# Kernel tuning notes

Hardware: AMD Instinct MI355X
Metric: run time of the kernel (lower is better)

The kernel has to match this reference:

```python
import jax, jax.numpy as jnp
import numpy as np

QUERY = 1024
VALUE = 1024
HID = 1024
SEQ = 2048
BATCH = 64
INIT_RANGE = 0.1


def setup_inputs() -> dict:
    key = jax.random.key(0)
    ks = jax.random.split(key, 5)
    q = jax.random.normal(ks[0], (BATCH, QUERY), dtype=jnp.float32)
    v = jax.random.normal(ks[1], (SEQ, BATCH, VALUE), dtype=jnp.float32)
    u = lambda k, shape: jax.random.uniform(k, shape, jnp.float32, -INIT_RANGE, INIT_RANGE)
    W_v = u(ks[2], (HID, VALUE))
    b_v = jnp.zeros((HID,), jnp.float32)
    W_q = u(ks[3], (HID, QUERY))
    b_q = jnp.zeros((HID,), jnp.float32)
    W_o = u(ks[4], (1, HID))
    b_o = jnp.zeros((1,), jnp.float32)
    return {"q": q, "v": v, "W_v": W_v, "b_v": b_v, "W_q": W_q, "b_q": b_q, "W_o": W_o, "b_o": b_o}


def reference(q, v, W_v, b_v, W_q, b_q, W_o, b_o):
    # v: [S, B, V] -> [B, S, V]
    vt = jnp.transpose(v, (1, 0, 2))
    h_v = jnp.einsum('bsv,hv->bsh', vt, W_v) + b_v          # [B, S, H]
    h_q = jnp.einsum('bq,hq->bh', q, W_q) + b_q              # [B, H]
    h = jnp.tanh(h_v + h_q[:, None, :])                      # [B, S, H]
    logit = jnp.einsum('bsh,h->bs', h, W_o[0]) + b_o[0]      # [B, S]
    logit = logit - jnp.max(logit, axis=1, keepdims=True)
    p = jax.nn.softmax(logit, axis=1)                        # [B, S]
    ctx = jnp.sum(vt * p[:, :, None], axis=1, keepdims=True) # [B, 1, V]
    out = jnp.transpose(ctx, (1, 0, 2))                      # [1, B, V]
    return (out, p)
```

## Files before the change

### kernel.cpp

```cpp
#include <hip/hip_runtime.h>
#include <hip/hip_bf16.h>
#include <stdint.h>

#define BATCH 64
#define SEQ   2048
#define VDIM  1024
#define HDIM  1024
#define LDSB  24576

typedef __bf16 b8v __attribute__((ext_vector_type(8)));
typedef __bf16 b4v __attribute__((ext_vector_type(4)));
typedef float f32x4 __attribute__((ext_vector_type(4)));
typedef unsigned short u16x8 __attribute__((ext_vector_type(8)));

__device__ __forceinline__ float bf2f(unsigned short u) {
    union { unsigned int i; float f; } cv; cv.i = ((unsigned int)u) << 16; return cv.f;
}

__device__ __forceinline__ unsigned int pack_bf16_2(float a, float b) {
#if __has_builtin(__builtin_amdgcn_cvt_pk_bf16_f32)
    auto t = __builtin_amdgcn_cvt_pk_bf16_f32(a, b);
    unsigned int r; __builtin_memcpy(&r, &t, 4); return r;
#else
    union { float f; unsigned int u; } ca, cb; ca.f = a; cb.f = b;
    unsigned int ra = ca.u + 0x7FFF + ((ca.u >> 16) & 1);
    unsigned int rb = cb.u + 0x7FFF + ((cb.u >> 16) & 1);
    return (ra >> 16) | (rb & 0xFFFF0000u);
#endif
}

__device__ __forceinline__ void gload_lds16(const unsigned short* g, unsigned short* l) {
    __builtin_amdgcn_global_load_lds(
        (const __attribute__((address_space(1))) unsigned int*)g,
        (__attribute__((address_space(3))) unsigned int*)l, 16, 0, 0);
}

__global__ __launch_bounds__(256) void cvt_bf16_kernel(
    const float* __restrict__ in, unsigned short* __restrict__ out, long n8)
{
    long g = (long)blockIdx.x * 256 + threadIdx.x;
    if (g >= n8) return;
    float4 a = *(const float4*)(in + g * 8);
    float4 b = *(const float4*)(in + g * 8 + 4);
    b8v o = {(__bf16)a.x, (__bf16)a.y, (__bf16)a.z, (__bf16)a.w,
             (__bf16)b.x, (__bf16)b.y, (__bf16)b.z, (__bf16)b.w};
    *(b8v*)(out + g * 8) = o;
}

__global__ __launch_bounds__(256) void hq_kernel(
    const float* __restrict__ q, const float* __restrict__ Wq,
    const float* __restrict__ bq, const float* __restrict__ bv,
    float* __restrict__ hq)
{
    const int h = blockIdx.x * 4 + (threadIdx.x >> 6);
    const int lane = threadIdx.x & 63;
    const float4* qr = (const float4*)(q + ((size_t)lane << 10));
    const float4* wr = (const float4*)(Wq + ((size_t)h << 10));
    float acc = 0.f;
    #pragma unroll 8
    for (int k = 0; k < 256; ++k) {
        float4 wa = wr[k];
        float4 qa = qr[k];
        acc += qa.x*wa.x + qa.y*wa.y + qa.z*wa.z + qa.w*wa.w;
    }
    hq[((size_t)lane << 10) + h] = acc + bq[h] + bv[h];
}

__global__ __launch_bounds__(512, 2) void fused_8ph(
    const unsigned short* __restrict__ v, const unsigned short* __restrict__ Wv,
    const float* __restrict__ Wo, const float* __restrict__ hq,
    float* __restrict__ logit)
{
    __shared__ __align__(16) unsigned short lds[3 * LDSB];
    __shared__ float logit_lds[128];

    const int tid  = threadIdx.x;
    const int w    = tid >> 6;
    const int lane = tid & 63;
    const int col  = lane & 15;
    const int quad = lane >> 4;
    const int wm   = w >> 2;
    const int wn   = w & 3;

    const int bid    = blockIdx.x;
    const int work   = ((bid & 7) << 9) + (bid >> 3);
    const int m_tile = work >> 2;
    const int n_tile = work & 3;

    if (tid < 128) logit_lds[tid] = 0.f;

    f32x4 acc[4][4];
    #pragma unroll
    for (int i = 0; i < 4; ++i)
        #pragma unroll
        for (int j = 0; j < 4; ++j) acc[i][j] = (f32x4)(0.f);

    const int rowoff = tid >> 3;
    const int ch     = (tid & 7) ^ (rowoff & 7);
    const unsigned short* gA = v  + (size_t)(m_tile * 128 + rowoff) * VDIM + (ch << 3);
    const unsigned short* gB = Wv + (size_t)(n_tile * 256 + rowoff) * VDIM + (ch << 3);
    const int ldA = tid << 3;
    const int ldB = 8192 + (tid << 3);

    gload_lds16(gA,                  lds + ldA);
    gload_lds16(gA + 64*VDIM,        lds + 4096 + ldA);
    gload_lds16(gB,                  lds + ldB);
    gload_lds16(gB + 64*VDIM,        lds + 4096 + ldB);
    gload_lds16(gB + 128*VDIM,       lds + 8192 + ldB);
    gload_lds16(gB + 192*VDIM,       lds + 12288 + ldB);
    gload_lds16(gA + 64,             lds + LDSB + ldA);
    gload_lds16(gA + 64 + 64*VDIM,   lds + LDSB + 4096 + ldA);
    gload_lds16(gB + 64,             lds + LDSB + ldB);
    gload_lds16(gB + 64 + 64*VDIM,   lds + LDSB + 4096 + ldB);
    gload_lds16(gB + 64 + 128*VDIM,  lds + LDSB + 8192 + ldB);
    gload_lds16(gB + 64 + 192*VDIM,  lds + LDSB + 12288 + ldB);
    asm volatile("s_waitcnt vmcnt(6)" ::: "memory");
    __builtin_amdgcn_s_barrier();

    const int aoffbase = (wm * 64 + col) * 64;
    const int boffbase = 8192 + (wn * 64 + col) * 64;
    const int axor     = col & 7;

    const unsigned short* gAs = gA + 128;
    const unsigned short* gBs = gB + 128;
    int cbase = 0;
    int sbase = 2 * LDSB;

    b8v aF[4], bF[4];

#define FRAG_LOAD(kkc)                                                          \
    {   const int co = ((((kkc) << 2) + quad) ^ axor) << 3;                     \
        _Pragma("unroll") for (int i = 0; i < 4; ++i)                           \
            aF[i] = *(const b8v*)(lds + cbase + aoffbase + i*1024 + co);        \
        _Pragma("unroll") for (int j = 0; j < 4; ++j)                           \
            bF[j] = *(const b8v*)(lds + cbase + boffbase + j*1024 + co);    }

#define MFMA16()                                                                \
    _Pragma("unroll") for (int i = 0; i < 4; ++i)                               \
        _Pragma("unroll") for (int j = 0; j < 4; ++j)                           \
            acc[i][j] = __builtin_amdgcn_mfma_f32_16x16x32_bf16(aF[i], bF[j], acc[i][j], 0, 0, 0);

    #pragma unroll 1
    for (int t = 0; t < 16; ++t) {
        FRAG_LOAD(0)
        if (t < 14) {
            gload_lds16(gAs,            lds + sbase + ldA);
            gload_lds16(gAs + 64*VDIM,  lds + sbase + 4096 + ldA);
            gload_lds16(gBs,            lds + sbase + ldB);
        }
        __builtin_amdgcn_s_barrier();
        asm volatile("s_waitcnt lgkmcnt(0)" ::: "memory");
        __builtin_amdgcn_sched_barrier(0);
        __builtin_amdgcn_s_setprio(1);
        MFMA16()
        __builtin_amdgcn_s_setprio(0);
        __builtin_amdgcn_s_barrier();

        FRAG_LOAD(1)
        if (t < 14) {
            gload_lds16(gBs + 64*VDIM,   lds + sbase + 4096 + ldB);
            gload_lds16(gBs + 128*VDIM,  lds + sbase + 8192 + ldB);
            gload_lds16(gBs + 192*VDIM,  lds + sbase + 12288 + ldB);
        }
        __builtin_amdgcn_s_barrier();
        asm volatile("s_waitcnt lgkmcnt(0)" ::: "memory");
        __builtin_amdgcn_sched_barrier(0);
        __builtin_amdgcn_s_setprio(1);
        MFMA16()
        __builtin_amdgcn_s_setprio(0);
        if (t <= 13)      { asm volatile("s_waitcnt vmcnt(6)" ::: "memory"); }
        else if (t == 14) { asm volatile("s_waitcnt vmcnt(0)" ::: "memory"); }
        __builtin_amdgcn_s_barrier();

        gAs += 64; gBs += 64;
        cbase += LDSB; if (cbase == 3 * LDSB) cbase = 0;
        sbase += LDSB; if (sbase == 3 * LDSB) sbase = 0;
    }
#undef FRAG_LOAD
#undef MFMA16

    float rowsum[4][4];
    #pragma unroll
    for (int i = 0; i < 4; ++i)
        #pragma unroll
        for (int r = 0; r < 4; ++r) rowsum[i][r] = 0.f;
    #pragma unroll
    for (int j = 0; j < 4; ++j) {
        const int h = n_tile * 256 + wn * 64 + j * 16 + col;
        const float wo = Wo[h];
        #pragma unroll
        for (int i = 0; i < 4; ++i) {
            const int brow = i * 16 + quad * 4;
            #pragma unroll
            for (int r = 0; r < 4; ++r) {
                float x = acc[i][j][r] + hq[(brow + r) * HDIM + h];
                float t = __expf(2.f * x);
                rowsum[i][r] += wo * (1.f - 2.f / (t + 1.f));
            }
        }
    }
    #pragma unroll
    for (int off = 1; off < 16; off <<= 1)
        #pragma unroll
        for (int i = 0; i < 4; ++i)
            #pragma unroll
            for (int r = 0; r < 4; ++r)
                rowsum[i][r] += __shfl_xor(rowsum[i][r], off, 64);
    if (col == 0) {
        #pragma unroll
        for (int i = 0; i < 4; ++i)
            #pragma unroll
            for (int r = 0; r < 4; ++r)
                atomicAdd(&logit_lds[wm * 64 + i * 16 + quad * 4 + r], rowsum[i][r]);
    }
    __syncthreads();
    if (tid < 128) {
        const int b = tid & 63;
        const int s = m_tile * 2 + (tid >> 6);
        atomicAdd(&logit[b * SEQ + s], logit_lds[tid]);
    }
}

#define GEMM_EPILOGUE()                                                        \
    float rowsum[4][4];                                                        \
    _Pragma("unroll") for (int i = 0; i < 4; ++i)                              \
        _Pragma("unroll") for (int r = 0; r < 4; ++r) rowsum[i][r] = 0.f;      \
    _Pragma("unroll") for (int j = 0; j < 4; ++j) {                            \
        const int h = n_tile*128 + wave_n + j*16 + col;                        \
        const float wo = Wo[h];                                                \
        _Pragma("unroll") for (int i = 0; i < 4; ++i) {                        \
            const int brow = i*16 + quad*4;                                    \
            _Pragma("unroll") for (int r = 0; r < 4; ++r) {                    \
                float x = acc[i][j][r] + hq[(brow + r)*HDIM + h];              \
                float t = __expf(2.f * x);                                     \
                rowsum[i][r] += wo * (1.f - 2.f / (t + 1.f));                  \
            }                                                                  \
        }                                                                      \
    }                                                                          \
    _Pragma("unroll") for (int off = 1; off < 16; off <<= 1)                   \
        _Pragma("unroll") for (int i = 0; i < 4; ++i)                          \
            _Pragma("unroll") for (int r = 0; r < 4; ++r)                      \
                rowsum[i][r] += __shfl_xor(rowsum[i][r], off, 64);             \
    if (col == 0) {                                                            \
        _Pragma("unroll") for (int i = 0; i < 4; ++i)                          \
            _Pragma("unroll") for (int r = 0; r < 4; ++r)                      \
                atomicAdd(&logit_lds[wave_m + i*16 + quad*4 + r], rowsum[i][r]); \
    }                                                                          \
    __syncthreads();                                                           \
    if (tid < 128) {                                                           \
        const int b = tid & 63;                                                \
        const int s = m_tile*2 + (tid >> 6);                                   \
        atomicAdd(&logit[b*SEQ + s], logit_lds[tid]);                          \
    }

__global__ __launch_bounds__(256) void fused_f32(
    const float* __restrict__ v, const float* __restrict__ Wv,
    const float* __restrict__ Wo, const float* __restrict__ hq,
    float* __restrict__ logit)
{
    __shared__ __align__(16) unsigned short ldsA[128*32];
    __shared__ __align__(16) unsigned short ldsB[128*32];
    __shared__ float logit_lds[128];

    const int tid  = threadIdx.x;
    const int w    = tid >> 6;
    const int lane = tid & 63;
    const int col  = lane & 15;
    const int quad = lane >> 4;
    const int wave_m = (w >> 1) << 6;
    const int wave_n = (w & 1) << 6;
    const int n_tile = blockIdx.x;
    const int m_tile = blockIdx.y;

    if (tid < 128) logit_lds[tid] = 0.f;

    f32x4 acc[4][4];
    #pragma unroll
    for (int i = 0; i < 4; ++i)
        #pragma unroll
        for (int j = 0; j < 4; ++j) acc[i][j] = (f32x4)(0.f);

    const int srow8 = lane >> 3;
    const int scolf = (lane & 7) << 2;
    const float* gA = v  + (size_t)(m_tile * 128 + w*32 + srow8) * VDIM + scolf;
    const float* gB = Wv + (size_t)(n_tile * 128 + w*32 + srow8) * VDIM + scolf;
    unsigned short* lA = ldsA + (w*32 + srow8)*32 + ((lane & 7) << 2);
    unsigned short* lB = ldsB + (w*32 + srow8)*32 + ((lane & 7) << 2);

    float4 ra[4], rb[4];
    #pragma unroll
    for (int r = 0; r < 4; ++r) {
        ra[r] = *(const float4*)(gA + r*8*VDIM);
        rb[r] = *(const float4*)(gB + r*8*VDIM);
    }

    for (int kt = 0; kt < 32; ++kt) {
        __syncthreads();
        #pragma unroll
        for (int r = 0; r < 4; ++r) {
            uint2 pa = { pack_bf16_2(ra[r].x, ra[r].y), pack_bf16_2(ra[r].z, ra[r].w) };
            uint2 pb = { pack_bf16_2(rb[r].x, rb[r].y), pack_bf16_2(rb[r].z, rb[r].w) };
            *(uint2*)(lA + r*256) = pa;
            *(uint2*)(lB + r*256) = pb;
        }
        __syncthreads();

        if (kt < 31) {
            const int ko = (kt + 1) << 5;
            #pragma unroll
            for (int r = 0; r < 4; ++r) {
                ra[r] = *(const float4*)(gA + ko + r*8*VDIM);
                rb[r] = *(const float4*)(gB + ko + r*8*VDIM);
            }
        }

        b8v aF[4], bF[4];
        #pragma unroll
        for (int i = 0; i < 4; ++i)
            aF[i] = *(const b8v*)(ldsA + ((wave_m + i*16 + col) << 5) + (quad << 3));
        #pragma unroll
        for (int j = 0; j < 4; ++j)
            bF[j] = *(const b8v*)(ldsB + ((wave_n + j*16 + col) << 5) + (quad << 3));
        #pragma unroll
        for (int i = 0; i < 4; ++i)
            #pragma unroll
            for (int j = 0; j < 4; ++j)
                acc[i][j] = __builtin_amdgcn_mfma_f32_16x16x32_bf16(aF[i], bF[j], acc[i][j], 0, 0, 0);
    }

    GEMM_EPILOGUE()
}

__global__ __launch_bounds__(256) void softmax_kernel(float* __restrict__ logit,
                                                      float* __restrict__ pout)
{
    const int b = blockIdx.x, tid = threadIdx.x;
    float* row = logit + b * SEQ;
    __shared__ float red[4];

    float e[8];
    float lmax = -1e30f;
    #pragma unroll
    for (int k = 0; k < 8; ++k) { e[k] = row[tid + k*256]; lmax = fmaxf(lmax, e[k]); }
    #pragma unroll
    for (int off = 32; off > 0; off >>= 1) lmax = fmaxf(lmax, __shfl_xor(lmax, off, 64));
    if ((tid & 63) == 0) red[tid >> 6] = lmax;
    __syncthreads();
    lmax = fmaxf(fmaxf(red[0], red[1]), fmaxf(red[2], red[3]));
    __syncthreads();
    float lsum = 0.f;
    #pragma unroll
    for (int k = 0; k < 8; ++k) { e[k] = __expf(e[k] - lmax); lsum += e[k]; }
    #pragma unroll
    for (int off = 32; off > 0; off >>= 1) lsum += __shfl_xor(lsum, off, 64);
    if ((tid & 63) == 0) red[tid >> 6] = lsum;
    __syncthreads();
    lsum = red[0] + red[1] + red[2] + red[3];
    const float inv = 1.f / lsum;
    #pragma unroll
    for (int k = 0; k < 8; ++k) {
        const int s = tid + k*256;
        const float pv = e[k] * inv;
        row[s] = pv;
        pout[b*SEQ + s] = pv;
    }
}

__global__ __launch_bounds__(128) void ctx_f32(
    const float* __restrict__ v, const float* __restrict__ p, float* __restrict__ ctx)
{
    const int b = blockIdx.y, sc = blockIdx.x, tid = threadIdx.x;
    float acc[8];
    #pragma unroll
    for (int e = 0; e < 8; ++e) acc[e] = 0.f;
    for (int s = sc*128; s < sc*128 + 128; ++s) {
        const float pv = p[b*SEQ + s];
        const float4* vp = (const float4*)(v + (size_t)(s*64 + b) * VDIM + tid*8);
        float4 v0 = vp[0], v1 = vp[1];
        acc[0] = fmaf(pv, v0.x, acc[0]); acc[1] = fmaf(pv, v0.y, acc[1]);
        acc[2] = fmaf(pv, v0.z, acc[2]); acc[3] = fmaf(pv, v0.w, acc[3]);
        acc[4] = fmaf(pv, v1.x, acc[4]); acc[5] = fmaf(pv, v1.y, acc[5]);
        acc[6] = fmaf(pv, v1.z, acc[6]); acc[7] = fmaf(pv, v1.w, acc[7]);
    }
    #pragma unroll
    for (int e = 0; e < 8; ++e) atomicAdd(&ctx[b*VDIM + tid*8 + e], acc[e]);
}

__global__ __launch_bounds__(128) void ctx_bf16(
    const unsigned short* __restrict__ v, const float* __restrict__ p, float* __restrict__ ctx)
{
    const int b = blockIdx.y, sc = blockIdx.x, tid = threadIdx.x;
    float acc[8];
    #pragma unroll
    for (int e = 0; e < 8; ++e) acc[e] = 0.f;
    for (int s = sc*128; s < sc*128 + 128; ++s) {
        const float pv = p[b*SEQ + s];
        u16x8 val = *(const u16x8*)(v + (size_t)(s*64 + b) * VDIM + tid*8);
        #pragma unroll
        for (int e = 0; e < 8; ++e) acc[e] = fmaf(pv, bf2f(val[e]), acc[e]);
    }
    #pragma unroll
    for (int e = 0; e < 8; ++e) atomicAdd(&ctx[b*VDIM + tid*8 + e], acc[e]);
}

extern "C" void kernel_launch(void* const* d_in, const int* in_sizes, int n_in,
                              void* d_out, int out_size, void* d_ws, size_t ws_size,
                              hipStream_t stream)
{
    const float* q  = (const float*)d_in[0];
    const float* v  = (const float*)d_in[1];
    const float* Wv = (const float*)d_in[2];
    const float* bv = (const float*)d_in[3];
    const float* Wq = (const float*)d_in[4];
    const float* bq = (const float*)d_in[5];
    const float* Wo = (const float*)d_in[6];

    float* hq_ws    = (float*)d_ws;
    float* logit_ws = hq_ws + 65536;
    float* ctx_ws   = logit_ws + 131072;
    unsigned short* vb  = (unsigned short*)(ctx_ws + 65536);
    unsigned short* Wvb = vb + (size_t)SEQ*BATCH*VDIM;

    const size_t needA = (size_t)(65536 + 131072 + 65536) * 4
                       + ((size_t)SEQ*BATCH*VDIM + (size_t)HDIM*VDIM) * 2;
    const bool bigws = ws_size >= needA;

    float* out_ctx = (float*)d_out;
    float* out_p   = out_ctx + 65536;

    hipMemsetAsync(logit_ws, 0, 131072 * sizeof(float), stream);
    hipMemsetAsync(out_ctx, 0, 65536 * sizeof(float), stream);
    hq_kernel<<<256, 256, 0, stream>>>(q, Wq, bq, bv, hq_ws);

    if (bigws) {
        cvt_bf16_kernel<<<65536, 256, 0, stream>>>(v,  vb,  (long)SEQ*BATCH*VDIM/8);
        cvt_bf16_kernel<<<512,   256, 0, stream>>>(Wv, Wvb, (long)HDIM*VDIM/8);
        fused_8ph<<<4096, 512, 0, stream>>>(vb, Wvb, Wo, hq_ws, logit_ws);
        softmax_kernel<<<64, 256, 0, stream>>>(logit_ws, out_p);
        ctx_bf16<<<dim3(16, 64), 128, 0, stream>>>(vb, logit_ws, out_ctx);
    } else {
        fused_f32<<<dim3(8, 1024), 256, 0, stream>>>(v, Wv, Wo, hq_ws, logit_ws);
        softmax_kernel<<<64, 256, 0, stream>>>(logit_ws, out_p);
        ctx_f32<<<dim3(16, 64), 128, 0, stream>>>(v, logit_ws, out_ctx);
    }
}
```

Before: 1.258 ms.

## Enlarge fused GEMM tile to 256x256 with BK=32 four-stage LDS pipeline

The fused v·Wv^T + tanh + Wo-reduction kernel moves from 128x256 tiles with a 3-stage 64-wide K pipeline to 256x256 tiles with a 4-stage 32-wide K pipeline, halving the grid and doubling accumulators per wave. This increases reuse of B fragments per LDS load and reduces global traffic for Wv. The tanh epilogue now uses a hardware reciprocal, the two memsets are merged into one, and ctx is accumulated in workspace then copied out. The change raises register pressure (32 accumulator tiles per wave) and LDS use to 128KB, which may limit occupancy despite launch bounds requesting two blocks.

Result: faster. 1.214 ms (-3.5%).

```diff
diff --git a/kernel.cpp b/kernel.cpp
--- a/kernel.cpp
+++ b/kernel.cpp
@@ -6,7 +6,6 @@
 #define SEQ   2048
 #define VDIM  1024
 #define HDIM  1024
-#define LDSB  24576
 
 typedef __bf16 b8v __attribute__((ext_vector_type(8)));
 typedef __bf16 b4v __attribute__((ext_vector_type(4)));
@@ -15,6 +14,15 @@
 
 __device__ __forceinline__ float bf2f(unsigned short u) {
     union { unsigned int i; float f; } cv; cv.i = ((unsigned int)u) << 16; return cv.f;
+}
+
+__device__ __forceinline__ float tanh_fast(float x) {
+    float t = __expf(2.f * x);
+#if __has_builtin(__builtin_amdgcn_rcpf)
+    return 1.f - 2.f * __builtin_amdgcn_rcpf(t + 1.f);
+#else
+    return 1.f - 2.f / (t + 1.f);
+#endif
 }
 
 __device__ __forceinline__ unsigned int pack_bf16_2(float a, float b) {
@@ -66,13 +74,13 @@
     hq[((size_t)lane << 10) + h] = acc + bq[h] + bv[h];
 }
 
-__global__ __launch_bounds__(512, 2) void fused_8ph(
+__global__ __launch_bounds__(512, 2) void fused_bk32(
     const unsigned short* __restrict__ v, const unsigned short* __restrict__ Wv,
     const float* __restrict__ Wo, const float* __restrict__ hq,
     float* __restrict__ logit)
 {
-    __shared__ __align__(16) unsigned short lds[3 * LDSB];
-    __shared__ float logit_lds[128];
+    __shared__ __align__(16) unsigned short lds[65536];
+    __shared__ float logit_lds[256];
 
     const int tid  = threadIdx.x;
     const int w    = tid >> 6;
@@ -83,105 +91,92 @@
     const int wn   = w & 3;
 
     const int bid    = blockIdx.x;
-    const int work   = ((bid & 7) << 9) + (bid >> 3);
+    const int work   = ((bid & 7) << 8) + (bid >> 3);
     const int m_tile = work >> 2;
     const int n_tile = work & 3;
 
-    if (tid < 128) logit_lds[tid] = 0.f;
-
-    f32x4 acc[4][4];
-    #pragma unroll
-    for (int i = 0; i < 4; ++i)
+    if (tid < 256) logit_lds[tid] = 0.f;
+
+    f32x4 acc[8][4];
+    #pragma unroll
+    for (int i = 0; i < 8; ++i)
         #pragma unroll
         for (int j = 0; j < 4; ++j) acc[i][j] = (f32x4)(0.f);
 
-    const int rowoff = tid >> 3;
-    const int ch     = (tid & 7) ^ (rowoff & 7);
-    const unsigned short* gA = v  + (size_t)(m_tile * 128 + rowoff) * VDIM + (ch << 3);
-    const unsigned short* gB = Wv + (size_t)(n_tile * 256 + rowoff) * VDIM + (ch << 3);
-    const int ldA = tid << 3;
-    const int ldB = 8192 + (tid << 3);
-
-    gload_lds16(gA,                  lds + ldA);
-    gload_lds16(gA + 64*VDIM,        lds + 4096 + ldA);
-    gload_lds16(gB,                  lds + ldB);
-    gload_lds16(gB + 64*VDIM,        lds + 4096 + ldB);
-    gload_lds16(gB + 128*VDIM,       lds + 8192 + ldB);
-    gload_lds16(gB + 192*VDIM,       lds + 12288 + ldB);
-    gload_lds16(gA + 64,             lds + LDSB + ldA);
-    gload_lds16(gA + 64 + 64*VDIM,   lds + LDSB + 4096 + ldA);
-    gload_lds16(gB + 64,             lds + LDSB + ldB);
-    gload_lds16(gB + 64 + 64*VDIM,   lds + LDSB + 4096 + ldB);
-    gload_lds16(gB + 64 + 128*VDIM,  lds + LDSB + 8192 + ldB);
-    gload_lds16(gB + 64 + 192*VDIM,  lds + LDSB + 12288 + ldB);
-    asm volatile("s_waitcnt vmcnt(6)" ::: "memory");
+    const int rA  = ((tid >> 6) << 4) + (tid & 15);
+    const int qch = (tid >> 4) & 3;
+    const unsigned short* gAs = v  + (size_t)(m_tile * 256 + rA) * VDIM + (qch << 3);
+    const unsigned short* gBs = Wv + (size_t)(n_tile * 256 + rA) * VDIM + (qch << 3);
+
+    {
+        unsigned short* d = lds + (tid << 3);
+        #pragma unroll
+        for (int pt = 0; pt < 3; ++pt) {
+            gload_lds16(gAs,             d);
+            gload_lds16(gAs + 128*VDIM,  d + 4096);
+            gload_lds16(gBs,             d + 8192);
+            gload_lds16(gBs + 128*VDIM,  d + 12288);
+            gAs += 32; gBs += 32; d += 16384;
+        }
+    }
+    asm volatile("s_waitcnt vmcnt(8)" ::: "memory");
     __builtin_amdgcn_s_barrier();
 
-    const int aoffbase = (wm * 64 + col) * 64;
-    const int boffbase = 8192 + (wn * 64 + col) * 64;
-    const int axor     = col & 7;
-
-    const unsigned short* gAs = gA + 128;
-    const unsigned short* gBs = gB + 128;
-    int cbase = 0;
-    int sbase = 2 * LDSB;
-
-    b8v aF[4], bF[4];
-
-#define FRAG_LOAD(kkc)                                                          \
-    {   const int co = ((((kkc) << 2) + quad) ^ axor) << 3;                     \
-        _Pragma("unroll") for (int i = 0; i < 4; ++i)                           \
-            aF[i] = *(const b8v*)(lds + cbase + aoffbase + i*1024 + co);        \
-        _Pragma("unroll") for (int j = 0; j < 4; ++j)                           \
-            bF[j] = *(const b8v*)(lds + cbase + boffbase + j*1024 + co);    }
-
-#define MFMA16()                                                                \
-    _Pragma("unroll") for (int i = 0; i < 4; ++i)                               \
-        _Pragma("unroll") for (int j = 0; j < 4; ++j)                           \
-            acc[i][j] = __builtin_amdgcn_mfma_f32_16x16x32_bf16(aF[i], bF[j], acc[i][j], 0, 0, 0);
+    const int aBase = (wm << 12) + (lane << 3);
+    const int bBase = 8192 + (wn << 11) + (lane << 3);
 
     #pragma unroll 1
-    for (int t = 0; t < 16; ++t) {
-        FRAG_LOAD(0)
-        if (t < 14) {
-            gload_lds16(gAs,            lds + sbase + ldA);
-            gload_lds16(gAs + 64*VDIM,  lds + sbase + 4096 + ldA);
-            gload_lds16(gBs,            lds + sbase + ldB);
+    for (int t = 0; t < 32; ++t) {
+        const unsigned short* bufp = lds + ((t & 3) << 14);
+        unsigned short* stp = lds + (((t + 3) & 3) << 14) + (tid << 3);
+        b8v aF[4], bF[4];
+
+        #pragma unroll
+        for (int j = 0; j < 4; ++j) bF[j] = *(const b8v*)(bufp + bBase + (j << 9));
+        #pragma unroll
+        for (int i = 0; i < 4; ++i) aF[i] = *(const b8v*)(bufp + aBase + (i << 9));
+        if (t <= 28) {
+            gload_lds16(gAs,            stp);
+            gload_lds16(gAs + 128*VDIM, stp + 4096);
         }
         __builtin_amdgcn_s_barrier();
         asm volatile("s_waitcnt lgkmcnt(0)" ::: "memory");
         __builtin_amdgcn_sched_barrier(0);
         __builtin_amdgcn_s_setprio(1);
-        MFMA16()
+        #pragma unroll
+        for (int i = 0; i < 4; ++i)
+            #pragma unroll
+            for (int j = 0; j < 4; ++j)
+                acc[i][j] = __builtin_amdgcn_mfma_f32_16x16x32_bf16(aF[i], bF[j], acc[i][j], 0, 0, 0);
         __builtin_amdgcn_s_setprio(0);
         __builtin_amdgcn_s_barrier();
 
-        FRAG_LOAD(1)
-        if (t < 14) {
-            gload_lds16(gBs + 64*VDIM,   lds + sbase + 4096 + ldB);
-            gload_lds16(gBs + 128*VDIM,  lds + sbase + 8192 + ldB);
-            gload_lds16(gBs + 192*VDIM,  lds + sbase + 12288 + ldB);
+        #pragma unroll
+        for (int i = 0; i < 4; ++i) aF[i] = *(const b8v*)(bufp + aBase + ((i + 4) << 9));
+        if (t <= 28) {
+            gload_lds16(gBs,            stp + 8192);
+            gload_lds16(gBs + 128*VDIM, stp + 12288);
+            gAs += 32; gBs += 32;
         }
         __builtin_amdgcn_s_barrier();
         asm volatile("s_waitcnt lgkmcnt(0)" ::: "memory");
         __builtin_amdgcn_sched_barrier(0);
         __builtin_amdgcn_s_setprio(1);
-        MFMA16()
+        #pragma unroll
+        for (int i = 0; i < 4; ++i)
+            #pragma unroll
+            for (int j = 0; j < 4; ++j)
+                acc[i + 4][j] = __builtin_amdgcn_mfma_f32_16x16x32_bf16(aF[i], bF[j], acc[i + 4][j], 0, 0, 0);
         __builtin_amdgcn_s_setprio(0);
-        if (t <= 13)      { asm volatile("s_waitcnt vmcnt(6)" ::: "memory"); }
-        else if (t == 14) { asm volatile("s_waitcnt vmcnt(0)" ::: "memory"); }
+        if (t < 29)       { asm volatile("s_waitcnt vmcnt(8)" ::: "memory"); }
+        else if (t == 29) { asm volatile("s_waitcnt vmcnt(4)" ::: "memory"); }
+        else if (t == 30) { asm volatile("s_waitcnt vmcnt(0)" ::: "memory"); }
         __builtin_amdgcn_s_barrier();
-
-        gAs += 64; gBs += 64;
-        cbase += LDSB; if (cbase == 3 * LDSB) cbase = 0;
-        sbase += LDSB; if (sbase == 3 * LDSB) sbase = 0;
-    }
-#undef FRAG_LOAD
-#undef MFMA16
-
-    float rowsum[4][4];
-    #pragma unroll
-    for (int i = 0; i < 4; ++i)
+    }
+
+    float rowsum[8][4];
+    #pragma unroll
+    for (int i = 0; i < 8; ++i)
         #pragma unroll
         for (int r = 0; r < 4; ++r) rowsum[i][r] = 0.f;
     #pragma unroll
@@ -190,33 +185,34 @@
         const float wo = Wo[h];
         #pragma unroll
         for (int i = 0; i < 4; ++i) {
-            const int brow = i * 16 + quad * 4;
             #pragma unroll
             for (int r = 0; r < 4; ++r) {
-                float x = acc[i][j][r] + hq[(brow + r) * HDIM + h];
-                float t = __expf(2.f * x);
-                rowsum[i][r] += wo * (1.f - 2.f / (t + 1.f));
+                const float hqv = hq[(i * 16 + quad * 4 + r) * HDIM + h];
+                float x0 = acc[i][j][r] + hqv;
+                float x1 = acc[i + 4][j][r] + hqv;
+                rowsum[i][r]     += wo * tanh_fast(x0);
+                rowsum[i + 4][r] += wo * tanh_fast(x1);
             }
         }
     }
     #pragma unroll
     for (int off = 1; off < 16; off <<= 1)
         #pragma unroll
-        for (int i = 0; i < 4; ++i)
+        for (int i = 0; i < 8; ++i)
             #pragma unroll
             for (int r = 0; r < 4; ++r)
                 rowsum[i][r] += __shfl_xor(rowsum[i][r], off, 64);
     if (col == 0) {
         #pragma unroll
-        for (int i = 0; i < 4; ++i)
+        for (int i = 0; i < 8; ++i)
             #pragma unroll
             for (int r = 0; r < 4; ++r)
-                atomicAdd(&logit_lds[wm * 64 + i * 16 + quad * 4 + r], rowsum[i][r]);
+                atomicAdd(&logit_lds[wm * 128 + i * 16 + quad * 4 + r], rowsum[i][r]);
     }
     __syncthreads();
-    if (tid < 128) {
+    if (tid < 256) {
         const int b = tid & 63;
-        const int s = m_tile * 2 + (tid >> 6);
+        const int s = m_tile * 4 + (tid >> 6);
         atomicAdd(&logit[b * SEQ + s], logit_lds[tid]);
     }
 }
@@ -403,6 +399,13 @@
     for (int e = 0; e < 8; ++e) atomicAdd(&ctx[b*VDIM + tid*8 + e], acc[e]);
 }
 
+__global__ __launch_bounds__(256) void copy_kernel(const float* __restrict__ src,
+                                                   float* __restrict__ dst)
+{
+    int g = blockIdx.x * 256 + threadIdx.x;
+    dst[g] = src[g];
+}
+
 extern "C" void kernel_launch(void* const* d_in, const int* in_sizes, int n_in,
                               void* d_out, int out_size, void* d_ws, size_t ws_size,
                               hipStream_t stream)
@@ -428,19 +431,19 @@
     float* out_ctx = (float*)d_out;
     float* out_p   = out_ctx + 65536;
 
-    hipMemsetAsync(logit_ws, 0, 131072 * sizeof(float), stream);
-    hipMemsetAsync(out_ctx, 0, 65536 * sizeof(float), stream);
+    hipMemsetAsync(logit_ws, 0, (131072 + 65536) * sizeof(float), stream);
     hq_kernel<<<256, 256, 0, stream>>>(q, Wq, bq, bv, hq_ws);
 
     if (bigws) {
         cvt_bf16_kernel<<<65536, 256, 0, stream>>>(v,  vb,  (long)SEQ*BATCH*VDIM/8);
         cvt_bf16_kernel<<<512,   256, 0, stream>>>(Wv, Wvb, (long)HDIM*VDIM/8);
-        fused_8ph<<<4096, 512, 0, stream>>>(vb, Wvb, Wo, hq_ws, logit_ws);
+        fused_bk32<<<2048, 512, 0, stream>>>(vb, Wvb, Wo, hq_ws, logit_ws);
         softmax_kernel<<<64, 256, 0, stream>>>(logit_ws, out_p);
-        ctx_bf16<<<dim3(16, 64), 128, 0, stream>>>(vb, logit_ws, out_ctx);
+        ctx_bf16<<<dim3(16, 64), 128, 0, stream>>>(vb, logit_ws, ctx_ws);
     } else {
         fused_f32<<<dim3(8, 1024), 256, 0, stream>>>(v, Wv, Wo, hq_ws, logit_ws);
         softmax_kernel<<<64, 256, 0, stream>>>(logit_ws, out_p);
-        ctx_f32<<<dim3(16, 64), 128, 0, stream>>>(v, logit_ws, out_ctx);
-    }
-}
+        ctx_f32<<<dim3(16, 64), 128, 0, stream>>>(v, logit_ws, ctx_ws);
+    }
+    copy_kernel<<<256, 256, 0, stream>>>(ctx_ws, out_ctx);
+}
```
